# Kernel tuning notes

Measured on AMD Instinct MI355X. Metric: run time of the kernel, lower is better.

The kernel has to match this reference:

```python
import jax, jax.numpy as jnp
import numpy as np

C = 256          # channels
G = 16           # dcn groups
K = 3            # dcn kernel size (P = K*K sampling points)
PAD = 1
DIL = 1
OFFSET_SCALE = 1.0
HIDDEN = 4 * C   # mlp_ratio = 4
EPS = 1e-6


def layer_norm(x, g, b):
    mu = x.mean(-1, keepdims=True)
    var = jnp.mean((x - mu) ** 2, -1, keepdims=True)
    return (x - mu) * jax.lax.rsqrt(var + EPS) * g + b


def grid_sample_bilinear(img, grid):
    """img: (B,Cg,H,W); grid: (B,L,P,2) xy in [-1,1].
    Matches F.grid_sample(mode='bilinear', padding_mode='zeros', align_corners=False)."""
    B, Cg, H, W = img.shape
    x = (grid[..., 0] + 1.0) * (W * 0.5) - 0.5
    y = (grid[..., 1] + 1.0) * (H * 0.5) - 0.5
    x0f = jnp.floor(x); y0f = jnp.floor(y)
    wx1 = x - x0f; wy1 = y - y0f
    x0 = x0f.astype(jnp.int32); y0 = y0f.astype(jnp.int32)
    flat = img.reshape(B, Cg, H * W)

    def tap(ix, iy, w):
        valid = (ix >= 0) & (ix < W) & (iy >= 0) & (iy < H)
        idx = jnp.clip(iy, 0, H - 1) * W + jnp.clip(ix, 0, W - 1)
        v = jnp.take_along_axis(flat, idx.reshape(B, 1, -1), axis=2)
        v = v.reshape(B, Cg, idx.shape[1], idx.shape[2])
        return v * (w * valid)[:, None]

    return (tap(x0, y0, (1 - wx1) * (1 - wy1))
            + tap(x0 + 1, y0, wx1 * (1 - wy1))
            + tap(x0, y0 + 1, (1 - wx1) * wy1)
            + tap(x0 + 1, y0 + 1, wx1 * wy1))


def dcnv3(x, dw_w, dw_b, off_w, off_b, mask_w, mask_b, inp_w, inp_b, out_w, out_b):
    """DCNv3 forward (dcnv3_core_pytorch math), x: (N,H,W,C) channels_last."""
    N, H, W, Cc = x.shape
    Cg = Cc // G
    P = K * K
    xp = x @ inp_w.T + inp_b                             # input_proj
    x1 = jax.lax.conv_general_dilated(
        x, dw_w, (1, 1), [(PAD, PAD), (PAD, PAD)],
        dimension_numbers=('NHWC', 'HWIO', 'NHWC'),
        feature_group_count=Cc) + dw_b                   # depthwise conv
    off = (x1 @ off_w.T + off_b).reshape(N, H, W, G, P, 2)
    m = jax.nn.softmax((x1 @ mask_w.T + mask_b).reshape(N, H, W, G, P), axis=-1)
    Hin, Win = H + 2 * PAD, W + 2 * PAD
    xpad = jnp.pad(xp, ((0, 0), (PAD, PAD), (PAD, PAD), (0, 0)))
    base = (DIL * (K - 1)) // 2
    ry = (jnp.arange(H, dtype=x.dtype) * 1.0 + base + 0.5) / Hin
    rx = (jnp.arange(W, dtype=x.dtype) * 1.0 + base + 0.5) / Win
    ref = jnp.stack([jnp.broadcast_to(rx[None, :], (H, W)),
                     jnp.broadcast_to(ry[:, None], (H, W))], -1)   # (H,W,2) xy
    xs = (jnp.arange(K, dtype=x.dtype) * DIL - base) / Win
    ys = (jnp.arange(K, dtype=x.dtype) * DIL - base) / Hin
    gx, gy = jnp.meshgrid(xs, ys, indexing='ij')         # w-major order as in torch ref
    grid = jnp.stack([gx, gy], -1).reshape(P, 2)
    norm = jnp.array([Win, Hin], dtype=x.dtype)
    loc = (ref[None, :, :, None, None, :] + grid * OFFSET_SCALE
           + off * (OFFSET_SCALE / norm))                # (N,H,W,G,P,2)
    sg = 2.0 * loc - 1.0
    img = xpad.reshape(N, Hin, Win, G, Cg).transpose(0, 3, 4, 1, 2).reshape(N * G, Cg, Hin, Win)
    sgr = sg.transpose(0, 3, 1, 2, 4, 5).reshape(N * G, H * W, P, 2)
    sampled = grid_sample_bilinear(img, sgr)             # (N*G,Cg,HW,P)
    mr = m.transpose(0, 3, 1, 2, 4).reshape(N * G, 1, H * W, P)
    out = (sampled * mr).sum(-1).reshape(N, G, Cg, H * W)
    out = out.transpose(0, 3, 1, 2).reshape(N, H, W, Cc)
    return out @ out_w.T + out_b                         # output_proj


def setup_inputs() -> dict:
    key = jax.random.key(0)
    ks = jax.random.split(key, 10)
    N, H, W = 8, 56, 56
    P = K * K

    def rn(k, shape, s):
        return jax.random.normal(k, shape, dtype=jnp.float32) * s

    return {
        'x': jax.random.normal(ks[0], (N, H, W, C), dtype=jnp.float32),
        'ln1_g': jnp.ones((C,), jnp.float32), 'ln1_b': jnp.zeros((C,), jnp.float32),
        'dw_w': rn(ks[1], (K, K, 1, C), 0.1), 'dw_b': jnp.zeros((C,), jnp.float32),
        'off_w': rn(ks[2], (G * P * 2, C), 0.02), 'off_b': jnp.zeros((G * P * 2,), jnp.float32),
        'mask_w': rn(ks[3], (G * P, C), 0.02), 'mask_b': jnp.zeros((G * P,), jnp.float32),
        'inp_w': rn(ks[4], (C, C), 0.05), 'inp_b': jnp.zeros((C,), jnp.float32),
        'out_w': rn(ks[5], (C, C), 0.05), 'out_b': jnp.zeros((C,), jnp.float32),
        'ln2_g': jnp.ones((C,), jnp.float32), 'ln2_b': jnp.zeros((C,), jnp.float32),
        'fc1_w': rn(ks[6], (HIDDEN, C), 0.05), 'fc1_b': jnp.zeros((HIDDEN,), jnp.float32),
        'fc2_w': rn(ks[7], (C, HIDDEN), 0.05), 'fc2_b': jnp.zeros((C,), jnp.float32),
    }


def reference(x, ln1_g, ln1_b, dw_w, dw_b, off_w, off_b, mask_w, mask_b,
              inp_w, inp_b, out_w, out_b, ln2_g, ln2_b, fc1_w, fc1_b, fc2_w, fc2_b):
    # pre-norm block, no layer_scale, drop_path=0
    y = x + dcnv3(layer_norm(x, ln1_g, ln1_b), dw_w, dw_b, off_w, off_b,
                  mask_w, mask_b, inp_w, inp_b, out_w, out_b)
    h = layer_norm(y, ln2_g, ln2_b)
    h = jax.nn.gelu(h @ fc1_w.T + fc1_b, approximate=False)
    return y + (h @ fc2_w.T + fc2_b)
```

## Files before the change

kernel.cpp:

```cpp
#include <hip/hip_runtime.h>
#include <hip/hip_bf16.h>
#include <math.h>

#define NTOK 25088
#define HW_  3136
#define HH   56
#define WW   56
#define CCH  256
#define NGRP 16
#define NPTS 9
#define HIDN 1024
#define NOFFM 432
#define TPB  4

typedef __attribute__((ext_vector_type(8))) __bf16 bf16x8;
typedef __attribute__((ext_vector_type(4))) __bf16 bf16x4;
typedef __attribute__((ext_vector_type(4))) float  f32x4;

static __device__ __forceinline__ void gl_lds16(const void* g, void* l) {
    __builtin_amdgcn_global_load_lds((const __attribute__((address_space(1))) void*)g,
                                     (__attribute__((address_space(3))) void*)l, 16, 0, 0);
}

static __device__ __forceinline__ float gelu_fast(float v) {
    float v2 = v * v;
    float z2 = fmaf(0.0713548163f * v, v2, 1.5957691216f * v);
    float r  = __builtin_amdgcn_rcpf(__expf(-z2) + 1.0f);
    return v * r;
}

__global__ __launch_bounds__(256)
void cvt_all_kernel(const float* __restrict__ inp_w, const float* __restrict__ out_w,
                    const float* __restrict__ off_w, const float* __restrict__ mask_w,
                    const float* __restrict__ fc1_w, const float* __restrict__ fc2_w,
                    const float* __restrict__ off_b, const float* __restrict__ mask_b,
                    __bf16* wib, __bf16* wob, __bf16* wcat, __bf16* w1b, __bf16* w2b,
                    float* bcat) {
    int i = blockIdx.x * 256 + threadIdx.x;
    if (i >= 191488) {
        int j = i - 191488;
        if (j < 432) bcat[j] = (j < 288) ? off_b[j] : mask_b[j - 288];
        return;
    }
    const float* s; __bf16* d; int off;
    if (i < 16384)       { s = inp_w;  d = wib;          off = i; }
    else if (i < 32768)  { s = out_w;  d = wob;          off = i - 16384; }
    else if (i < 51200)  { s = off_w;  d = wcat;         off = i - 32768; }
    else if (i < 60416)  { s = mask_w; d = wcat + 73728; off = i - 51200; }
    else if (i < 125952) { s = fc1_w;  d = w1b;          off = i - 60416; }
    else                 { s = fc2_w;  d = w2b;          off = i - 125952; }
    float4 v = ((const float4*)s)[off];
    bf16x4 o = {(__bf16)v.x, (__bf16)v.y, (__bf16)v.z, (__bf16)v.w};
    ((bf16x4*)d)[off] = o;
}

__global__ __launch_bounds__(256)
void ln_kernel(const float* __restrict__ x, const float* __restrict__ g,
               const float* __restrict__ b, __bf16* __restrict__ outb, int ntok) {
    int gid  = blockIdx.x * 256 + threadIdx.x;
    int t    = gid >> 6;
    int lane = threadIdx.x & 63;
    if (t >= ntok) return;
    float4 v = ((const float4*)(x + (size_t)t * CCH))[lane];
    float s = v.x + v.y + v.z + v.w;
#pragma unroll
    for (int o = 1; o < 64; o <<= 1) s += __shfl_xor(s, o);
    float mu = s * 0.00390625f;
    float dx = v.x - mu, dy = v.y - mu, dz = v.z - mu, dw = v.w - mu;
    float q = dx * dx + dy * dy + dz * dz + dw * dw;
#pragma unroll
    for (int o = 1; o < 64; o <<= 1) q += __shfl_xor(q, o);
    float rstd = rsqrtf(q * 0.00390625f + 1e-6f);
    float4 gg = ((const float4*)g)[lane];
    float4 bb = ((const float4*)b)[lane];
    bf16x4 ob = {(__bf16)(dx * rstd * gg.x + bb.x), (__bf16)(dy * rstd * gg.y + bb.y),
                 (__bf16)(dz * rstd * gg.z + bb.z), (__bf16)(dw * rstd * gg.w + bb.w)};
    ((bf16x4*)(outb + (size_t)t * CCH))[lane] = ob;
}

__global__ __launch_bounds__(256)
void dwconv_kernel(const __bf16* __restrict__ ln, const float* __restrict__ wt,
                   const float* __restrict__ bias, __bf16* __restrict__ out) {
    int gid = blockIdx.x * 256 + threadIdx.x;
    int t = gid >> 6;
    int cq = gid & 63;
    if (t >= NTOK) return;
    int n = t / HW_, hw = t % HW_;
    int h = hw / WW, w0 = hw % WW;
    float4 a = ((const float4*)bias)[cq];
    const bf16x4* l4 = (const bf16x4*)ln;
    const float4* w4 = (const float4*)wt;
#pragma unroll
    for (int ky = 0; ky < 3; ++ky) {
        int y = h + ky - 1;
        if (y < 0 || y >= HH) continue;
#pragma unroll
        for (int kx = 0; kx < 3; ++kx) {
            int x = w0 + kx - 1;
            if (x < 0 || x >= WW) continue;
            bf16x4 v = l4[(size_t)(n * HW_ + y * WW + x) * 64 + cq];
            float4 ww = w4[(ky * 3 + kx) * 64 + cq];
            a.x += (float)v[0] * ww.x; a.y += (float)v[1] * ww.y;
            a.z += (float)v[2] * ww.z; a.w += (float)v[3] * ww.w;
        }
    }
    bf16x4 ob = {(__bf16)a.x, (__bf16)a.y, (__bf16)a.z, (__bf16)a.w};
    ((bf16x4*)out)[(size_t)t * 64 + cq] = ob;
}

template <int EPI>
__global__ __launch_bounds__(256, 6)
void gemm_kernel(const __bf16* __restrict__ A, const __bf16* __restrict__ W,
                 const float* __restrict__ bias, const float* __restrict__ resid,
                 float* __restrict__ outf, __bf16* __restrict__ outb,
                 const int Ndim, const int Kdim, const int NB) {
    __shared__ __align__(16) __bf16 Alds[2][64 * 32];
    __shared__ __align__(16) __bf16 Blds[2][128 * 32];

    const int tid  = threadIdx.x;
    const int w    = tid >> 6;
    const int lane = tid & 63;
    const int chunk = gridDim.x >> 3;
    const int lin   = (blockIdx.x & 7) * chunk + (blockIdx.x >> 3);
    const int m0 = (lin / NB) * 64;
    const int n0 = (lin % NB) * 128;
    const int wr = (w >> 1) * 32;
    const int wc = (w & 1) * 64;

    f32x4 acc[2][4];
#pragma unroll
    for (int i = 0; i < 2; ++i)
#pragma unroll
        for (int j = 0; j < 4; ++j) acc[i][j] = (f32x4){0.f, 0.f, 0.f, 0.f};

    const int pA   = tid;
    const int arow = pA >> 2, abyte = ((pA & 3) ^ ((pA >> 4) & 3)) * 16;
    const int pB1  = tid + 256;
    const int br0  = tid >> 2, br1 = pB1 >> 2;
    int bR0 = n0 + ((br0 >> 6) << 6) + 4 * (br0 & 15) + ((br0 >> 4) & 3);
    int bR1 = n0 + ((br1 >> 6) << 6) + 4 * (br1 & 15) + ((br1 >> 4) & 3);
    if (bR0 > Ndim - 1) bR0 = Ndim - 1;
    if (bR1 > Ndim - 1) bR1 = Ndim - 1;
    const int bb0 = ((tid & 3) ^ ((tid >> 3) & 3)) * 16;
    const int bb1 = ((pB1 & 3) ^ ((pB1 >> 3) & 3)) * 16;

    const char* Ab = (const char*)A;
    const char* Wb = (const char*)W;
    char* AL = (char*)&Alds[0][0];
    char* BL = (char*)&Blds[0][0];
    const size_t rb  = (size_t)Kdim * 2;
    const size_t sA  = (size_t)(m0 + arow) * rb + abyte;
    const size_t sB0 = (size_t)bR0 * rb + bb0;
    const size_t sB1 = (size_t)bR1 * rb + bb1;
    const int dof = w * 1024;

#define STAGE(BUF, KB)                                                 \
    do {                                                               \
        gl_lds16(Ab + sA  + (KB), AL + (BUF) * 4096 + dof);            \
        gl_lds16(Wb + sB0 + (KB), BL + (BUF) * 8192 + dof);            \
        gl_lds16(Wb + sB1 + (KB), BL + (BUF) * 8192 + 4096 + dof);     \
    } while (0)

    const int mrow = lane & 15;
    const int q    = lane >> 4;
    const int kA   = ((q ^ (mrow >> 2)) & 3) * 16;
    const int kB   = ((q ^ (mrow >> 1)) & 3) * 16;

    int cur = 0;
    STAGE(0, 0);
    __syncthreads();
    for (int k0 = 0; k0 < Kdim; k0 += 32) {
        const bool more = (k0 + 32 < Kdim);
        if (more) STAGE(cur ^ 1, (size_t)(k0 + 32) * 2);
        bf16x8 af[2], bfr[4];
#pragma unroll
        for (int i = 0; i < 2; ++i)
            af[i] = *(const bf16x8*)(AL + cur * 4096 + (wr + i * 16 + mrow) * 64 + kA);
#pragma unroll
        for (int i = 0; i < 4; ++i)
            bfr[i] = *(const bf16x8*)(BL + cur * 8192 + (wc + i * 16 + mrow) * 64 + kB);
#pragma unroll
        for (int mi = 0; mi < 2; ++mi)
#pragma unroll
            for (int ni = 0; ni < 4; ++ni)
                acc[mi][ni] = __builtin_amdgcn_mfma_f32_16x16x32_bf16(af[mi], bfr[ni], acc[mi][ni], 0, 0, 0);
        if (more) {
            __syncthreads();
            cur ^= 1;
        }
    }
#undef STAGE

    const int coll = lane & 15;
    const int rowh = (lane >> 4) * 4;
    const int col0 = n0 + wc + 4 * coll;
    if (col0 < Ndim) {
        const float4 bv = *(const float4*)(bias + col0);
#pragma unroll
        for (int mi = 0; mi < 2; ++mi) {
#pragma unroll
            for (int j = 0; j < 4; ++j) {
                const int row = m0 + wr + mi * 16 + rowh + j;
                const size_t idx = (size_t)row * (size_t)Ndim + col0;
                float4 v = make_float4(acc[mi][0][j] + bv.x, acc[mi][1][j] + bv.y,
                                       acc[mi][2][j] + bv.z, acc[mi][3][j] + bv.w);
                if (EPI == 1) {
                    const float4 r = *(const float4*)(resid + idx);
                    v.x += r.x; v.y += r.y; v.z += r.z; v.w += r.w;
                    *(float4*)(outf + idx) = v;
                } else if (EPI == 2) {
                    bf16x4 ob = {(__bf16)gelu_fast(v.x), (__bf16)gelu_fast(v.y),
                                 (__bf16)gelu_fast(v.z), (__bf16)gelu_fast(v.w)};
                    *(bf16x4*)(outb + idx) = ob;
                } else {
                    bf16x4 ob = {(__bf16)v.x, (__bf16)v.y, (__bf16)v.z, (__bf16)v.w};
                    *(bf16x4*)(outb + idx) = ob;
                }
            }
        }
    }
}

__global__ __launch_bounds__(256)
void dcn_kernel(const __bf16* __restrict__ xp, const __bf16* __restrict__ om,
                __bf16* __restrict__ out) {
    __shared__ float  raw[TPB][NOFFM];
    __shared__ int4   sidx[NPTS][TPB * NGRP];
    __shared__ float4 swt[NPTS][TPB * NGRP];
    const int tid = threadIdx.x;
    const int bid = blockIdx.x;
    const int b   = (bid & 7) * 784 + (bid >> 3);
    const int t0  = b * TPB;

    if (tid < (TPB * NOFFM) / 8) {
        bf16x8 v = *(const bf16x8*)(om + (size_t)t0 * NOFFM + tid * 8);
        float* d = &raw[0][0] + tid * 8;
#pragma unroll
        for (int k = 0; k < 8; ++k) d[k] = (float)v[k];
    }
    __syncthreads();

    if (tid < TPB * NGRP) {
        const int lt = tid >> 4, g = tid & 15;
        float* m = &raw[lt][288 + g * 9];
        float mx = m[0];
#pragma unroll
        for (int p = 1; p < 9; ++p) mx = fmaxf(mx, m[p]);
        float s = 0.f, e[9];
#pragma unroll
        for (int p = 0; p < 9; ++p) { e[p] = __expf(m[p] - mx); s += e[p]; }
        const float inv = 1.f / s;
#pragma unroll
        for (int p = 0; p < 9; ++p) m[p] = e[p] * inv;
    }
    __syncthreads();

    for (int e = tid; e < TPB * NGRP * NPTS; e += 256) {
        const int lt = e / 144, r = e % 144, g = r / 9, p = r % 9;
        const int t  = t0 + lt;
        const int hw = t % HW_;
        const int h = hw / WW, w0 = hw % WW;
        const float offx = raw[lt][g * 18 + p * 2 + 0];
        const float offy = raw[lt][g * 18 + p * 2 + 1];
        const float pm   = raw[lt][288 + g * 9 + p];
        const int kx = p / 3, ky = p % 3;
        const float fx = (float)(w0 + kx - 1) + offx;
        const float fy = (float)(h  + ky - 1) + offy;
        const float x0f = floorf(fx), y0f = floorf(fy);
        const float wx = fx - x0f, wy = fy - y0f;
        const int x0 = (int)x0f, y0 = (int)y0f;
        const bool xv0 = (unsigned)x0 < WW, xv1 = (unsigned)(x0 + 1) < WW;
        const bool yv0 = (unsigned)y0 < HH, yv1 = (unsigned)(y0 + 1) < HH;
        const int xc0 = min(max(x0, 0), WW - 1), xc1 = min(max(x0 + 1, 0), WW - 1);
        const int yc0 = min(max(y0, 0), HH - 1), yc1 = min(max(y0 + 1, 0), HH - 1);
        const int tg = lt * 16 + g;
        sidx[p][tg] = make_int4(yc0 * WW + xc0, yc0 * WW + xc1, yc1 * WW + xc0, yc1 * WW + xc1);
        swt[p][tg]  = make_float4((xv0 && yv0) ? (1.f - wx) * (1.f - wy) * pm : 0.f,
                                  (xv1 && yv0) ? wx * (1.f - wy) * pm : 0.f,
                                  (xv0 && yv1) ? (1.f - wx) * wy * pm : 0.f,
                                  (xv1 && yv1) ? wx * wy * pm : 0.f);
    }
    __syncthreads();

    const int lt = tid >> 6, lane = tid & 63;
    const int g = lane >> 2;
    const int t = t0 + lt;
    const int n = t / HW_;
    const int tg = lt * 16 + g;
    const __bf16* base = xp + (size_t)n * HW_ * CCH + lane * 4;
    f32x4 acc = {0.f, 0.f, 0.f, 0.f};
#pragma unroll
    for (int p = 0; p < NPTS; ++p) {
        const int4   id = sidx[p][tg];
        const float4 wv = swt[p][tg];
        bf16x4 v0 = *(const bf16x4*)(base + (size_t)id.x * CCH);
        bf16x4 v1 = *(const bf16x4*)(base + (size_t)id.y * CCH);
        bf16x4 v2 = *(const bf16x4*)(base + (size_t)id.z * CCH);
        bf16x4 v3 = *(const bf16x4*)(base + (size_t)id.w * CCH);
#pragma unroll
        for (int k = 0; k < 4; ++k)
            acc[k] += wv.x * (float)v0[k] + wv.y * (float)v1[k]
                    + wv.z * (float)v2[k] + wv.w * (float)v3[k];
    }
    bf16x4 ob = {(__bf16)acc[0], (__bf16)acc[1], (__bf16)acc[2], (__bf16)acc[3]};
    ((bf16x4*)out)[(size_t)t * 64 + lane] = ob;
}

extern "C" void kernel_launch(void* const* d_in, const int* in_sizes, int n_in,
                              void* d_out, int out_size, void* d_ws, size_t ws_size,
                              hipStream_t stream) {
    const float* x      = (const float*)d_in[0];
    const float* ln1_g  = (const float*)d_in[1];
    const float* ln1_b  = (const float*)d_in[2];
    const float* dw_w   = (const float*)d_in[3];
    const float* dw_b   = (const float*)d_in[4];
    const float* off_w  = (const float*)d_in[5];
    const float* off_b  = (const float*)d_in[6];
    const float* mask_w = (const float*)d_in[7];
    const float* mask_b = (const float*)d_in[8];
    const float* inp_w  = (const float*)d_in[9];
    const float* inp_b  = (const float*)d_in[10];
    const float* out_w  = (const float*)d_in[11];
    const float* out_b  = (const float*)d_in[12];
    const float* ln2_g  = (const float*)d_in[13];
    const float* ln2_b  = (const float*)d_in[14];
    const float* fc1_w  = (const float*)d_in[15];
    const float* fc1_b  = (const float*)d_in[16];
    const float* fc2_w  = (const float*)d_in[17];
    const float* fc2_b  = (const float*)d_in[18];
    float* out = (float*)d_out;

    char* ws = (char*)d_ws;
    size_t o = 0;
    auto alloc = [&](size_t bytes) { size_t r = o; o += (bytes + 255) & ~(size_t)255; return r; };
    float*  yf    = (float*)(ws + alloc((size_t)NTOK * CCH * 4));
    __bf16* x1b   = (__bf16*)(ws + alloc((size_t)NTOK * CCH * 2));
    __bf16* lnb   = (__bf16*)(ws + alloc((size_t)NTOK * CCH * 2));
    __bf16* xpb   = (__bf16*)(ws + alloc((size_t)NTOK * CCH * 2));
    __bf16* offmb = (__bf16*)(ws + alloc((size_t)NTOK * NOFFM * 2));
    alloc(4 * 1024 * 1024);
    __bf16* wib   = (__bf16*)(ws + alloc((size_t)65536 * 2));
    __bf16* wob   = (__bf16*)(ws + alloc((size_t)65536 * 2));
    __bf16* wcat  = (__bf16*)(ws + alloc((size_t)110592 * 2));
    __bf16* w1b   = (__bf16*)(ws + alloc((size_t)262144 * 2));
    __bf16* w2b   = (__bf16*)(ws + alloc((size_t)262144 * 2));
    float*  bcat  = (float*)(ws + alloc((size_t)432 * 4));
    if (ws_size < o) return;

    __bf16* dcnb = lnb;
    __bf16* l2b  = x1b;
    __bf16* h1b  = lnb;

    cvt_all_kernel<<<750, 256, 0, stream>>>(inp_w, out_w, off_w, mask_w, fc1_w, fc2_w,
                                            off_b, mask_b, wib, wob, wcat, w1b, w2b, bcat);

    ln_kernel<<<NTOK / 4, 256, 0, stream>>>(x, ln1_g, ln1_b, lnb, NTOK);
    dwconv_kernel<<<NTOK / 4, 256, 0, stream>>>(lnb, dw_w, dw_b, x1b);
    gemm_kernel<3><<<392 * 4, 256, 0, stream>>>(x1b, wcat, bcat, nullptr, nullptr, offmb, NOFFM, 256, 4);
    gemm_kernel<3><<<392 * 2, 256, 0, stream>>>(lnb, wib, inp_b, nullptr, nullptr, xpb, 256, 256, 2);
    dcn_kernel<<<NTOK / TPB, 256, 0, stream>>>(xpb, offmb, dcnb);
    gemm_kernel<1><<<392 * 2, 256, 0, stream>>>(dcnb, wob, out_b, x, yf, nullptr, 256, 256, 2);
    ln_kernel<<<NTOK / 4, 256, 0, stream>>>(yf, ln2_g, ln2_b, l2b, NTOK);
    gemm_kernel<2><<<392 * 8, 256, 0, stream>>>(l2b, w1b, fc1_b, nullptr, nullptr, h1b, 1024, 256, 8);
    gemm_kernel<1><<<392 * 2, 256, 0, stream>>>(h1b, w2b, fc2_b, yf, out, nullptr, 256, 1024, 2);
}
```

Measured before the change: 183.0 us.

## Merge offset/input-proj GEMMs, store residual in bf16, widen DCN gather vectors

The offset/mask GEMM and the input-projection GEMM now run in one launch that splits blocks by index. The intermediate residual y is stored as bf16 instead of fp32, which cuts its write and two reads, but it adds rounding error to the residual path. The DCN kernel now handles 8 tokens per block with 8-wide bf16 gathers per lane. It keeps offsets in LDS as bf16 and stores sample indices as ushort to reduce LDS footprint.

```diff
diff --git a/kernel.cpp b/kernel.cpp
--- a/kernel.cpp
+++ b/kernel.cpp
@@ -11,7 +11,7 @@
 #define NPTS 9
 #define HIDN 1024
 #define NOFFM 432
-#define TPB  4
+#define TPB  8
 
 typedef __attribute__((ext_vector_type(8))) __bf16 bf16x8;
 typedef __attribute__((ext_vector_type(4))) __bf16 bf16x4;
@@ -55,18 +55,43 @@
 }
 
 __global__ __launch_bounds__(256)
-void ln_kernel(const float* __restrict__ x, const float* __restrict__ g,
-               const float* __restrict__ b, __bf16* __restrict__ outb, int ntok) {
+void ln_f_kernel(const float* __restrict__ x, const float* __restrict__ g,
+                 const float* __restrict__ b, __bf16* __restrict__ outb) {
     int gid  = blockIdx.x * 256 + threadIdx.x;
     int t    = gid >> 6;
     int lane = threadIdx.x & 63;
-    if (t >= ntok) return;
+    if (t >= NTOK) return;
     float4 v = ((const float4*)(x + (size_t)t * CCH))[lane];
     float s = v.x + v.y + v.z + v.w;
 #pragma unroll
     for (int o = 1; o < 64; o <<= 1) s += __shfl_xor(s, o);
     float mu = s * 0.00390625f;
     float dx = v.x - mu, dy = v.y - mu, dz = v.z - mu, dw = v.w - mu;
+    float q = dx * dx + dy * dy + dz * dz + dw * dw;
+#pragma unroll
+    for (int o = 1; o < 64; o <<= 1) q += __shfl_xor(q, o);
+    float rstd = rsqrtf(q * 0.00390625f + 1e-6f);
+    float4 gg = ((const float4*)g)[lane];
+    float4 bb = ((const float4*)b)[lane];
+    bf16x4 ob = {(__bf16)(dx * rstd * gg.x + bb.x), (__bf16)(dy * rstd * gg.y + bb.y),
+                 (__bf16)(dz * rstd * gg.z + bb.z), (__bf16)(dw * rstd * gg.w + bb.w)};
+    ((bf16x4*)(outb + (size_t)t * CCH))[lane] = ob;
+}
+
+__global__ __launch_bounds__(256)
+void ln_b_kernel(const __bf16* __restrict__ x, const float* __restrict__ g,
+                 const float* __restrict__ b, __bf16* __restrict__ outb) {
+    int gid  = blockIdx.x * 256 + threadIdx.x;
+    int t    = gid >> 6;
+    int lane = threadIdx.x & 63;
+    if (t >= NTOK) return;
+    bf16x4 vb = ((const bf16x4*)(x + (size_t)t * CCH))[lane];
+    float vx = (float)vb[0], vy = (float)vb[1], vz = (float)vb[2], vw = (float)vb[3];
+    float s = vx + vy + vz + vw;
+#pragma unroll
+    for (int o = 1; o < 64; o <<= 1) s += __shfl_xor(s, o);
+    float mu = s * 0.00390625f;
+    float dx = vx - mu, dy = vy - mu, dz = vz - mu, dw = vw - mu;
     float q = dx * dx + dy * dy + dz * dz + dw * dw;
 #pragma unroll
     for (int o = 1; o < 64; o <<= 1) q += __shfl_xor(q, o);
@@ -109,19 +134,18 @@
 }
 
 template <int EPI>
-__global__ __launch_bounds__(256, 6)
-void gemm_kernel(const __bf16* __restrict__ A, const __bf16* __restrict__ W,
-                 const float* __restrict__ bias, const float* __restrict__ resid,
-                 float* __restrict__ outf, __bf16* __restrict__ outb,
-                 const int Ndim, const int Kdim, const int NB) {
+static __device__ __forceinline__ void gemm_body(
+        const __bf16* __restrict__ A, const __bf16* __restrict__ W,
+        const float* __restrict__ bias, const float* __restrict__ residf,
+        const __bf16* __restrict__ residb, float* __restrict__ outf,
+        __bf16* __restrict__ outb, const int Ndim, const int Kdim,
+        const int NB, const int lin) {
     __shared__ __align__(16) __bf16 Alds[2][64 * 32];
     __shared__ __align__(16) __bf16 Blds[2][128 * 32];
 
     const int tid  = threadIdx.x;
     const int w    = tid >> 6;
     const int lane = tid & 63;
-    const int chunk = gridDim.x >> 3;
-    const int lin   = (blockIdx.x & 7) * chunk + (blockIdx.x >> 3);
     const int m0 = (lin / NB) * 64;
     const int n0 = (lin % NB) * 128;
     const int wr = (w >> 1) * 32;
@@ -204,54 +228,83 @@
                 const size_t idx = (size_t)row * (size_t)Ndim + col0;
                 float4 v = make_float4(acc[mi][0][j] + bv.x, acc[mi][1][j] + bv.y,
                                        acc[mi][2][j] + bv.z, acc[mi][3][j] + bv.w);
-                if (EPI == 1) {
-                    const float4 r = *(const float4*)(resid + idx);
-                    v.x += r.x; v.y += r.y; v.z += r.z; v.w += r.w;
-                    *(float4*)(outf + idx) = v;
-                } else if (EPI == 2) {
+                if (EPI == 2) {
                     bf16x4 ob = {(__bf16)gelu_fast(v.x), (__bf16)gelu_fast(v.y),
                                  (__bf16)gelu_fast(v.z), (__bf16)gelu_fast(v.w)};
                     *(bf16x4*)(outb + idx) = ob;
-                } else {
+                } else if (EPI == 3) {
                     bf16x4 ob = {(__bf16)v.x, (__bf16)v.y, (__bf16)v.z, (__bf16)v.w};
                     *(bf16x4*)(outb + idx) = ob;
+                } else if (EPI == 4) {
+                    const float4 r = *(const float4*)(residf + idx);
+                    bf16x4 ob = {(__bf16)(v.x + r.x), (__bf16)(v.y + r.y),
+                                 (__bf16)(v.z + r.z), (__bf16)(v.w + r.w)};
+                    *(bf16x4*)(outb + idx) = ob;
+                } else {
+                    const bf16x4 r = *(const bf16x4*)(residb + idx);
+                    v.x += (float)r[0]; v.y += (float)r[1];
+                    v.z += (float)r[2]; v.w += (float)r[3];
+                    *(float4*)(outf + idx) = v;
                 }
             }
         }
     }
 }
 
+template <int EPI>
+__global__ __launch_bounds__(256, 6)
+void gemm_kernel(const __bf16* __restrict__ A, const __bf16* __restrict__ W,
+                 const float* __restrict__ bias, const float* __restrict__ residf,
+                 const __bf16* __restrict__ residb, float* __restrict__ outf,
+                 __bf16* __restrict__ outb, const int Ndim, const int Kdim, const int NB) {
+    const int chunk = gridDim.x >> 3;
+    const int lin   = (blockIdx.x & 7) * chunk + (blockIdx.x >> 3);
+    gemm_body<EPI>(A, W, bias, residf, residb, outf, outb, Ndim, Kdim, NB, lin);
+}
+
+__global__ __launch_bounds__(256, 6)
+void gemm_dual_kernel(const __bf16* __restrict__ A1, const __bf16* __restrict__ W1,
+                      const float* __restrict__ b1, __bf16* __restrict__ o1,
+                      const int N1, const int NB1, const int split,
+                      const __bf16* __restrict__ A2, const __bf16* __restrict__ W2,
+                      const float* __restrict__ b2, __bf16* __restrict__ o2,
+                      const int N2, const int NB2) {
+    const int chunk = gridDim.x >> 3;
+    const int lin   = (blockIdx.x & 7) * chunk + (blockIdx.x >> 3);
+    if (lin < split)
+        gemm_body<3>(A1, W1, b1, nullptr, nullptr, nullptr, o1, N1, 256, NB1, lin);
+    else
+        gemm_body<3>(A2, W2, b2, nullptr, nullptr, nullptr, o2, N2, 256, NB2, lin - split);
+}
+
 __global__ __launch_bounds__(256)
 void dcn_kernel(const __bf16* __restrict__ xp, const __bf16* __restrict__ om,
                 __bf16* __restrict__ out) {
-    __shared__ float  raw[TPB][NOFFM];
-    __shared__ int4   sidx[NPTS][TPB * NGRP];
-    __shared__ float4 swt[NPTS][TPB * NGRP];
+    __shared__ __align__(16) __bf16 rawb[TPB][NOFFM];
+    __shared__ ushort4 sidx[NPTS][TPB * NGRP];
+    __shared__ float4  swt[NPTS][TPB * NGRP];
     const int tid = threadIdx.x;
     const int bid = blockIdx.x;
-    const int b   = (bid & 7) * 784 + (bid >> 3);
+    const int b   = (bid & 7) * 392 + (bid >> 3);
     const int t0  = b * TPB;
 
-    if (tid < (TPB * NOFFM) / 8) {
-        bf16x8 v = *(const bf16x8*)(om + (size_t)t0 * NOFFM + tid * 8);
-        float* d = &raw[0][0] + tid * 8;
-#pragma unroll
-        for (int k = 0; k < 8; ++k) d[k] = (float)v[k];
-    }
+    for (int e = tid; e < (TPB * NOFFM) / 8; e += 256)
+        *(bf16x8*)(&rawb[0][0] + e * 8) = *(const bf16x8*)(om + (size_t)t0 * NOFFM + e * 8);
     __syncthreads();
 
     if (tid < TPB * NGRP) {
         const int lt = tid >> 4, g = tid & 15;
-        float* m = &raw[lt][288 + g * 9];
-        float mx = m[0];
-#pragma unroll
-        for (int p = 1; p < 9; ++p) mx = fmaxf(mx, m[p]);
-        float s = 0.f, e[9];
-#pragma unroll
-        for (int p = 0; p < 9; ++p) { e[p] = __expf(m[p] - mx); s += e[p]; }
+        __bf16* m = &rawb[lt][288 + g * 9];
+        float e[9];
+        float mx = -1e30f;
+#pragma unroll
+        for (int p = 0; p < 9; ++p) { e[p] = (float)m[p]; mx = fmaxf(mx, e[p]); }
+        float s = 0.f;
+#pragma unroll
+        for (int p = 0; p < 9; ++p) { e[p] = __expf(e[p] - mx); s += e[p]; }
         const float inv = 1.f / s;
 #pragma unroll
-        for (int p = 0; p < 9; ++p) m[p] = e[p] * inv;
+        for (int p = 0; p < 9; ++p) m[p] = (__bf16)(e[p] * inv);
     }
     __syncthreads();
 
@@ -260,9 +313,9 @@
         const int t  = t0 + lt;
         const int hw = t % HW_;
         const int h = hw / WW, w0 = hw % WW;
-        const float offx = raw[lt][g * 18 + p * 2 + 0];
-        const float offy = raw[lt][g * 18 + p * 2 + 1];
-        const float pm   = raw[lt][288 + g * 9 + p];
+        const float offx = (float)rawb[lt][g * 18 + p * 2 + 0];
+        const float offy = (float)rawb[lt][g * 18 + p * 2 + 1];
+        const float pm   = (float)rawb[lt][288 + g * 9 + p];
         const int kx = p / 3, ky = p % 3;
         const float fx = (float)(w0 + kx - 1) + offx;
         const float fy = (float)(h  + ky - 1) + offy;
@@ -274,7 +327,10 @@
         const int xc0 = min(max(x0, 0), WW - 1), xc1 = min(max(x0 + 1, 0), WW - 1);
         const int yc0 = min(max(y0, 0), HH - 1), yc1 = min(max(y0 + 1, 0), HH - 1);
         const int tg = lt * 16 + g;
-        sidx[p][tg] = make_int4(yc0 * WW + xc0, yc0 * WW + xc1, yc1 * WW + xc0, yc1 * WW + xc1);
+        sidx[p][tg] = make_ushort4((unsigned short)(yc0 * WW + xc0),
+                                   (unsigned short)(yc0 * WW + xc1),
+                                   (unsigned short)(yc1 * WW + xc0),
+                                   (unsigned short)(yc1 * WW + xc1));
         swt[p][tg]  = make_float4((xv0 && yv0) ? (1.f - wx) * (1.f - wy) * pm : 0.f,
                                   (xv1 && yv0) ? wx * (1.f - wy) * pm : 0.f,
                                   (xv0 && yv1) ? (1.f - wx) * wy * pm : 0.f,
@@ -282,28 +338,30 @@
     }
     __syncthreads();
 
-    const int lt = tid >> 6, lane = tid & 63;
-    const int g = lane >> 2;
+    const int lt = tid >> 5, lane = tid & 31;
+    const int g = lane >> 1;
     const int t = t0 + lt;
     const int n = t / HW_;
     const int tg = lt * 16 + g;
-    const __bf16* base = xp + (size_t)n * HW_ * CCH + lane * 4;
-    f32x4 acc = {0.f, 0.f, 0.f, 0.f};
+    const __bf16* base = xp + (size_t)n * HW_ * CCH + lane * 8;
+    float acc[8] = {0.f, 0.f, 0.f, 0.f, 0.f, 0.f, 0.f, 0.f};
 #pragma unroll
     for (int p = 0; p < NPTS; ++p) {
-        const int4   id = sidx[p][tg];
-        const float4 wv = swt[p][tg];
-        bf16x4 v0 = *(const bf16x4*)(base + (size_t)id.x * CCH);
-        bf16x4 v1 = *(const bf16x4*)(base + (size_t)id.y * CCH);
-        bf16x4 v2 = *(const bf16x4*)(base + (size_t)id.z * CCH);
-        bf16x4 v3 = *(const bf16x4*)(base + (size_t)id.w * CCH);
-#pragma unroll
-        for (int k = 0; k < 4; ++k)
+        const ushort4 id = sidx[p][tg];
+        const float4  wv = swt[p][tg];
+        bf16x8 v0 = *(const bf16x8*)(base + (size_t)id.x * CCH);
+        bf16x8 v1 = *(const bf16x8*)(base + (size_t)id.y * CCH);
+        bf16x8 v2 = *(const bf16x8*)(base + (size_t)id.z * CCH);
+        bf16x8 v3 = *(const bf16x8*)(base + (size_t)id.w * CCH);
+#pragma unroll
+        for (int k = 0; k < 8; ++k)
             acc[k] += wv.x * (float)v0[k] + wv.y * (float)v1[k]
                     + wv.z * (float)v2[k] + wv.w * (float)v3[k];
     }
-    bf16x4 ob = {(__bf16)acc[0], (__bf16)acc[1], (__bf16)acc[2], (__bf16)acc[3]};
-    ((bf16x4*)out)[(size_t)t * 64 + lane] = ob;
+    bf16x8 ob;
+#pragma unroll
+    for (int k = 0; k < 8; ++k) ob[k] = (__bf16)acc[k];
+    *(bf16x8*)(out + (size_t)t * CCH + lane * 8) = ob;
 }
 
 extern "C" void kernel_launch(void* const* d_in, const int* in_sizes, int n_in,
@@ -333,12 +391,12 @@
     char* ws = (char*)d_ws;
     size_t o = 0;
     auto alloc = [&](size_t bytes) { size_t r = o; o += (bytes + 255) & ~(size_t)255; return r; };
-    float*  yf    = (float*)(ws + alloc((size_t)NTOK * CCH * 4));
+    __bf16* yb    = (__bf16*)(ws + alloc((size_t)NTOK * CCH * 2));
     __bf16* x1b   = (__bf16*)(ws + alloc((size_t)NTOK * CCH * 2));
     __bf16* lnb   = (__bf16*)(ws + alloc((size_t)NTOK * CCH * 2));
     __bf16* xpb   = (__bf16*)(ws + alloc((size_t)NTOK * CCH * 2));
     __bf16* offmb = (__bf16*)(ws + alloc((size_t)NTOK * NOFFM * 2));
-    alloc(4 * 1024 * 1024);
+    alloc(6 * 1024 * 1024);
     __bf16* wib   = (__bf16*)(ws + alloc((size_t)65536 * 2));
     __bf16* wob   = (__bf16*)(ws + alloc((size_t)65536 * 2));
     __bf16* wcat  = (__bf16*)(ws + alloc((size_t)110592 * 2));
@@ -354,13 +412,14 @@
     cvt_all_kernel<<<750, 256, 0, stream>>>(inp_w, out_w, off_w, mask_w, fc1_w, fc2_w,
                                             off_b, mask_b, wib, wob, wcat, w1b, w2b, bcat);
 
-    ln_kernel<<<NTOK / 4, 256, 0, stream>>>(x, ln1_g, ln1_b, lnb, NTOK);
+    ln_f_kernel<<<NTOK / 4, 256, 0, stream>>>(x, ln1_g, ln1_b, lnb);
     dwconv_kernel<<<NTOK / 4, 256, 0, stream>>>(lnb, dw_w, dw_b, x1b);
-    gemm_kernel<3><<<392 * 4, 256, 0, stream>>>(x1b, wcat, bcat, nullptr, nullptr, offmb, NOFFM, 256, 4);
-    gemm_kernel<3><<<392 * 2, 256, 0, stream>>>(lnb, wib, inp_b, nullptr, nullptr, xpb, 256, 256, 2);
+    gemm_dual_kernel<<<392 * 4 + 392 * 2, 256, 0, stream>>>(
+        x1b, wcat, bcat, offmb, NOFFM, 4, 392 * 4,
+        lnb, wib, inp_b, xpb, 256, 2);
     dcn_kernel<<<NTOK / TPB, 256, 0, stream>>>(xpb, offmb, dcnb);
-    gemm_kernel<1><<<392 * 2, 256, 0, stream>>>(dcnb, wob, out_b, x, yf, nullptr, 256, 256, 2);
-    ln_kernel<<<NTOK / 4, 256, 0, stream>>>(yf, ln2_g, ln2_b, l2b, NTOK);
-    gemm_kernel<2><<<392 * 8, 256, 0, stream>>>(l2b, w1b, fc1_b, nullptr, nullptr, h1b, 1024, 256, 8);
-    gemm_kernel<1><<<392 * 2, 256, 0, stream>>>(h1b, w2b, fc2_b, yf, out, nullptr, 256, 1024, 2);
-}
+    gemm_kernel<4><<<392 * 2, 256, 0, stream>>>(dcnb, wob, out_b, x, nullptr, nullptr, yb, 256, 256, 2);
+    ln_b_kernel<<<NTOK / 4, 256, 0, stream>>>(yb, ln2_g, ln2_b, l2b);
+    gemm_kernel<2><<<392 * 8, 256, 0, stream>>>(l2b, w1b, fc1_b, nullptr, nullptr, nullptr, h1b, 1024, 256, 8);
+    gemm_kernel<5><<<392 * 2, 256, 0, stream>>>(h1b, w2b, fc2_b, nullptr, yb, out, nullptr, 256, 1024, 2);
+}
```

New measurement: 171.9 us. 1.06x faster.
